# Performance work log

Hardware: AMD Instinct MI355X
Metric: run time of the kernel (lower is better)

The kernel has to match this reference:

```python
import jax, jax.numpy as jnp
import numpy as np

# Single-device reference: with head-parallel world size 1, both _SeqAllToAll
# collectives are identities, so the forward is exactly the kv-packed causal
# attention computed by loongtrain_attn_kvpacked_func (flash-attn semantics).

def setup_inputs() -> dict:
    key = jax.random.key(0)
    k1, k2 = jax.random.split(key)
    B, S, H, D = 1, 2048, 32, 128
    q = jax.random.normal(k1, (B, S, H, D), dtype=jnp.float32)
    kv = jax.random.normal(k2, (B, S, 2, H, D), dtype=jnp.float32)
    return {"q": q, "kv": kv}


def reference(q, kv) -> jnp.ndarray:
    # q: [B, S, H, D]; kv: [B, S, 2, H, D] (flash-attn kvpacked layout)
    B, S, H, D = q.shape
    k = kv[:, :, 0]  # [B, S, H, D]
    v = kv[:, :, 1]  # [B, S, H, D]
    scale = 1.0 / jnp.sqrt(jnp.asarray(D, dtype=q.dtype))
    # scores: [B, H, Sq, Sk]
    scores = jnp.einsum("bshd,bthd->bhst", q, k) * scale
    # causal mask (LoongTrain attention is causal)
    causal = jnp.tril(jnp.ones((S, S), dtype=bool))
    scores = jnp.where(causal[None, None, :, :], scores, jnp.asarray(-jnp.inf, dtype=scores.dtype))
    probs = jax.nn.softmax(scores, axis=-1)
    # context: [B, S, H, D]
    context = jnp.einsum("bhst,bthd->bshd", probs, v)
    return context
```

## Files before the change

kernel.cpp:

```cpp
#include <hip/hip_runtime.h>
#include <hip/hip_bf16.h>

typedef __bf16 bf16_t;
typedef __bf16 bf16x4 __attribute__((ext_vector_type(4)));
typedef __bf16 bf16x8 __attribute__((ext_vector_type(8)));
typedef float  f32x4  __attribute__((ext_vector_type(4)));

constexpr int S  = 2048;
constexpr int H  = 32;
constexpr int D  = 128;
constexpr int BR = 128;
constexpr int SC = 32;
constexpr int NT = S / BR;
constexpr int KSTR  = 136;
constexpr int VSTR2 = 20;

__device__ __forceinline__ bf16x8 cvt8(f32x4 lo, f32x4 hi) {
    bf16x8 r;
#pragma unroll
    for (int j = 0; j < 4; ++j) { r[j] = (bf16_t)lo[j]; r[4 + j] = (bf16_t)hi[j]; }
    return r;
}
__device__ __forceinline__ uint32_t pk2(float a, float b) {
    union { uint32_t u; bf16_t h[2]; } r;
    r.h[0] = (bf16_t)a; r.h[1] = (bf16_t)b;
    return r.u;
}

__global__ __launch_bounds__(256, 2)
void fa_fwd(const float* __restrict__ q, const float* __restrict__ kvp,
            float* __restrict__ out) {
    __shared__ __align__(16) bf16_t   Klds[2][SC * KSTR];
    __shared__ __align__(16) uint32_t Vt2[2][D * VSTR2];

    const int bx = blockIdx.x;
    const int h  = bx & 31;
    const int i  = bx >> 5;
    const int qtile = (i < 8) ? (15 - i) : (i - 8);
    const int q0    = qtile * BR;

    const int t    = threadIdx.x;
    const int w    = t >> 6;
    const int lane = t & 63;
    const int quad = lane >> 4;
    const int m    = lane & 15;

    const float sc = 0.08838834764831845f * 1.44269504088896340f;

    const int k2 = t >> 4, kc = t & 15;
    const int r0 = 2 * k2;
    const int lr0 = ((r0 >> 3) << 2) + (r0 & 3) + ((r0 & 4) ? 16 : 0);
    const size_t rowstep = (size_t)2 * H * D;
    const size_t tstep   = (size_t)SC * rowstep;
    const float* pk = kvp + (((size_t)r0 * 2 + 0) * H + h) * D + kc * 8;
    const float* pv = kvp + (((size_t)r0 * 2 + 1) * H + h) * D + kc * 8;
    const int vpos = k2 ^ ((kc & 3) << 2);

    const int qp0   = q0 + w * 32 + m;
    const int nkv   = (qtile + 1) * (BR / SC);
    const int qmaxw = q0 + w * 32 + 31;

    bf16x8 aq[2][4];
#pragma unroll
    for (int g = 0; g < 2; ++g)
#pragma unroll
        for (int c = 0; c < 4; ++c) {
            const float* p = q + ((size_t)(qp0 + g * 16) * H + h) * D + c * 32 + quad * 8;
            f32x4 lo = *(const f32x4*)p * sc;
            f32x4 hi = *(const f32x4*)(p + 4) * sc;
            aq[g][c] = cvt8(lo, hi);
        }

    f32x4 o[2][8];
#pragma unroll
    for (int g = 0; g < 2; ++g)
#pragma unroll
        for (int idx = 0; idx < 8; ++idx) o[g][idx] = (f32x4)0.f;
    float lrow[2] = {0.f, 0.f};

    f32x4 kr[2][2], vr[2][2];
    auto ldregs = [&]() {
        kr[0][0] = *(const f32x4*)pk;             kr[0][1] = *(const f32x4*)(pk + 4);
        kr[1][0] = *(const f32x4*)(pk + rowstep); kr[1][1] = *(const f32x4*)(pk + rowstep + 4);
        vr[0][0] = *(const f32x4*)pv;             vr[0][1] = *(const f32x4*)(pv + 4);
        vr[1][0] = *(const f32x4*)(pv + rowstep); vr[1][1] = *(const f32x4*)(pv + rowstep + 4);
    };
    auto stage = [&](int b) {
        *(bf16x8*)&Klds[b][lr0       * KSTR + kc * 8] = cvt8(kr[0][0], kr[0][1]);
        *(bf16x8*)&Klds[b][(lr0 + 1) * KSTR + kc * 8] = cvt8(kr[1][0], kr[1][1]);
#pragma unroll
        for (int j = 0; j < 8; ++j) {
            const int d = kc * 8 + j;
            const float a  = (j < 4) ? vr[0][0][j] : vr[0][1][j - 4];
            const float bb = (j < 4) ? vr[1][0][j] : vr[1][1][j - 4];
            Vt2[b][d * VSTR2 + vpos] = pk2(a, bb);
        }
    };

    ldregs();
    stage(0);
    if (nkv > 1) { pk += tstep; pv += tstep; ldregs(); }
    __syncthreads();

    for (int kb = 0; kb < nkv; ++kb) {
        const int kv0 = kb * SC;
        const int cur = kb & 1;
        const bool active = (kv0 <= qmaxw);

        bf16x8 bp0, bp1, av[8];
        if (active) {
            f32x4 sA[2][2];
#pragma unroll
            for (int g = 0; g < 2; ++g) { sA[g][0] = (f32x4)0.f; sA[g][1] = (f32x4)0.f; }
            __builtin_amdgcn_s_setprio(1);
#pragma unroll
            for (int c = 0; c < 4; ++c) {
                bf16x8 ak0 = *(const bf16x8*)&Klds[cur][m * KSTR + c * 32 + quad * 8];
                bf16x8 ak1 = *(const bf16x8*)&Klds[cur][(16 + m) * KSTR + c * 32 + quad * 8];
                sA[0][0] = __builtin_amdgcn_mfma_f32_16x16x32_bf16(ak0, aq[0][c], sA[0][0], 0, 0, 0);
                sA[0][1] = __builtin_amdgcn_mfma_f32_16x16x32_bf16(ak1, aq[0][c], sA[0][1], 0, 0, 0);
                sA[1][0] = __builtin_amdgcn_mfma_f32_16x16x32_bf16(ak0, aq[1][c], sA[1][0], 0, 0, 0);
                sA[1][1] = __builtin_amdgcn_mfma_f32_16x16x32_bf16(ak1, aq[1][c], sA[1][1], 0, 0, 0);
            }
            __builtin_amdgcn_s_setprio(0);

#pragma unroll
            for (int tt = 0; tt < 8; ++tt) {
                const int dd  = tt * 16 + m;
                const int grp = quad ^ ((dd >> 3) & 3);
                av[tt] = *(const bf16x8*)&Vt2[cur][dd * VSTR2 + grp * 4];
            }

#pragma unroll
            for (int g = 0; g < 2; ++g) {
                const int limb = q0 + w * 32 + g * 16 - kv0;
                float p[8], rs = 0.f;
                if (limb >= 31) {
#pragma unroll
                    for (int r = 0; r < 4; ++r) {
                        p[r]     = __builtin_amdgcn_exp2f(fminf(sA[g][0][r], 80.f));
                        p[4 + r] = __builtin_amdgcn_exp2f(fminf(sA[g][1][r], 80.f));
                        rs += p[r] + p[4 + r];
                    }
                } else {
                    const int lim = limb + m;
#pragma unroll
                    for (int r = 0; r < 4; ++r) {
                        float e0 = __builtin_amdgcn_exp2f(fminf(sA[g][0][r], 80.f));
                        float e1 = __builtin_amdgcn_exp2f(fminf(sA[g][1][r], 80.f));
                        p[r]     = (quad * 8 + r     <= lim) ? e0 : 0.f;
                        p[4 + r] = (quad * 8 + 4 + r <= lim) ? e1 : 0.f;
                        rs += p[r] + p[4 + r];
                    }
                }
                lrow[g] += rs;
                bf16x8 bv;
#pragma unroll
                for (int r = 0; r < 4; ++r) { bv[r] = (bf16_t)p[r]; bv[4 + r] = (bf16_t)p[4 + r]; }
                if (g == 0) bp0 = bv; else bp1 = bv;
            }
        }

        if (kb + 1 < nkv) {
            stage(cur ^ 1);
            if (kb + 2 < nkv) { pk += tstep; pv += tstep; ldregs(); }
        }

        if (active) {
            __builtin_amdgcn_s_setprio(1);
#pragma unroll
            for (int tt = 0; tt < 8; ++tt) {
                o[0][tt] = __builtin_amdgcn_mfma_f32_16x16x32_bf16(av[tt], bp0, o[0][tt], 0, 0, 0);
                o[1][tt] = __builtin_amdgcn_mfma_f32_16x16x32_bf16(av[tt], bp1, o[1][tt], 0, 0, 0);
            }
            __builtin_amdgcn_s_setprio(0);
        }
        __syncthreads();
    }

#pragma unroll
    for (int g = 0; g < 2; ++g) {
        lrow[g] += __shfl_xor(lrow[g], 16);
        lrow[g] += __shfl_xor(lrow[g], 32);
    }

#pragma unroll
    for (int g = 0; g < 2; ++g) {
        const float inv = 1.0f / lrow[g];
        float* op = out + ((size_t)(qp0 + g * 16) * H + h) * D;
#pragma unroll
        for (int tt = 0; tt < 8; ++tt) {
            f32x4 val = o[g][tt] * inv;
            *(f32x4*)(op + tt * 16 + quad * 4) = val;
        }
    }
}

extern "C" void kernel_launch(void* const* d_in, const int* in_sizes, int n_in,
                              void* d_out, int out_size, void* d_ws, size_t ws_size,
                              hipStream_t stream) {
    const float* q  = (const float*)d_in[0];
    const float* kv = (const float*)d_in[1];
    float* out = (float*)d_out;
    dim3 grid(NT * H);
    dim3 block(256);
    fa_fwd<<<grid, block, 0, stream>>>(q, kv, out);
}
```

Measured before the change: 176.9 us.

## Halve query tile to 64 rows, one 16-row group per wave, raise occupancy

Shrinks the query tile from 128 to 64 rows, so each wave handles a single 16-row group. This doubles the grid and allows four blocks per CU, with a new four-group interleaved tile order to balance causal work. V fragments are now loaded from LDS just before the PV MFMAs instead of being held in registers. The V transpose stores are also reordered by column half, which looks aimed at avoiding LDS bank conflicts. In exchange, each K/V chunk is reloaded and converted from fp32 by twice as many blocks, doubling global K/V traffic and staging work per unit of compute.

Measured after the change: 190.8 us. 1.08x slower.

```diff
diff --git a/kernel.cpp b/kernel.cpp
--- a/kernel.cpp
+++ b/kernel.cpp
@@ -9,7 +9,7 @@
 constexpr int S  = 2048;
 constexpr int H  = 32;
 constexpr int D  = 128;
-constexpr int BR = 128;
+constexpr int BR = 64;
 constexpr int SC = 32;
 constexpr int NT = S / BR;
 constexpr int KSTR  = 136;
@@ -27,7 +27,7 @@
     return r.u;
 }
 
-__global__ __launch_bounds__(256, 2)
+__global__ __launch_bounds__(256, 4)
 void fa_fwd(const float* __restrict__ q, const float* __restrict__ kvp,
             float* __restrict__ out) {
     __shared__ __align__(16) bf16_t   Klds[2][SC * KSTR];
@@ -36,7 +36,9 @@
     const int bx = blockIdx.x;
     const int h  = bx & 31;
     const int i  = bx >> 5;
-    const int qtile = (i < 8) ? (15 - i) : (i - 8);
+    const int jg = i & 7, gi = i >> 3;
+    const int qtile = (gi == 0) ? (31 - jg) : (gi == 1) ? jg
+                     : (gi == 2) ? (23 - jg) : (8 + jg);
     const int q0    = qtile * BR;
 
     const int t    = threadIdx.x;
@@ -55,28 +57,25 @@
     const float* pk = kvp + (((size_t)r0 * 2 + 0) * H + h) * D + kc * 8;
     const float* pv = kvp + (((size_t)r0 * 2 + 1) * H + h) * D + kc * 8;
     const int vpos = k2 ^ ((kc & 3) << 2);
+    const bool hb  = (kc & 4) != 0;
 
-    const int qp0   = q0 + w * 32 + m;
+    const int qp0   = q0 + w * 16 + m;
     const int nkv   = (qtile + 1) * (BR / SC);
-    const int qmaxw = q0 + w * 32 + 31;
+    const int qmaxw = q0 + w * 16 + 15;
 
-    bf16x8 aq[2][4];
+    bf16x8 aq[4];
 #pragma unroll
-    for (int g = 0; g < 2; ++g)
+    for (int c = 0; c < 4; ++c) {
+        const float* p = q + ((size_t)qp0 * H + h) * D + c * 32 + quad * 8;
+        f32x4 lo = *(const f32x4*)p * sc;
+        f32x4 hi = *(const f32x4*)(p + 4) * sc;
+        aq[c] = cvt8(lo, hi);
+    }
+
+    f32x4 o[8];
 #pragma unroll
-        for (int c = 0; c < 4; ++c) {
-            const float* p = q + ((size_t)(qp0 + g * 16) * H + h) * D + c * 32 + quad * 8;
-            f32x4 lo = *(const f32x4*)p * sc;
-            f32x4 hi = *(const f32x4*)(p + 4) * sc;
-            aq[g][c] = cvt8(lo, hi);
-        }
-
-    f32x4 o[2][8];
-#pragma unroll
-    for (int g = 0; g < 2; ++g)
-#pragma unroll
-        for (int idx = 0; idx < 8; ++idx) o[g][idx] = (f32x4)0.f;
-    float lrow[2] = {0.f, 0.f};
+    for (int idx = 0; idx < 8; ++idx) o[idx] = (f32x4)0.f;
+    float lrow = 0.f;
 
     f32x4 kr[2][2], vr[2][2];
     auto ldregs = [&]() {
@@ -88,12 +87,16 @@
     auto stage = [&](int b) {
         *(bf16x8*)&Klds[b][lr0       * KSTR + kc * 8] = cvt8(kr[0][0], kr[0][1]);
         *(bf16x8*)&Klds[b][(lr0 + 1) * KSTR + kc * 8] = cvt8(kr[1][0], kr[1][1]);
+        f32x4 aA = hb ? vr[0][1] : vr[0][0];
+        f32x4 bA = hb ? vr[1][1] : vr[1][0];
+        f32x4 aB = hb ? vr[0][0] : vr[0][1];
+        f32x4 bB = hb ? vr[1][0] : vr[1][1];
+        const int dA = kc * 8 + (hb ? 4 : 0);
+        const int dB = kc * 8 + (hb ? 0 : 4);
 #pragma unroll
-        for (int j = 0; j < 8; ++j) {
-            const int d = kc * 8 + j;
-            const float a  = (j < 4) ? vr[0][0][j] : vr[0][1][j - 4];
-            const float bb = (j < 4) ? vr[1][0][j] : vr[1][1][j - 4];
-            Vt2[b][d * VSTR2 + vpos] = pk2(a, bb);
+        for (int jq = 0; jq < 4; ++jq) {
+            Vt2[b][(dA + jq) * VSTR2 + vpos] = pk2(aA[jq], bA[jq]);
+            Vt2[b][(dB + jq) * VSTR2 + vpos] = pk2(aB[jq], bB[jq]);
         }
     };
 
@@ -107,58 +110,43 @@
         const int cur = kb & 1;
         const bool active = (kv0 <= qmaxw);
 
-        bf16x8 bp0, bp1, av[8];
+        bf16x8 bp;
         if (active) {
-            f32x4 sA[2][2];
-#pragma unroll
-            for (int g = 0; g < 2; ++g) { sA[g][0] = (f32x4)0.f; sA[g][1] = (f32x4)0.f; }
+            f32x4 sA[2];
+            sA[0] = (f32x4)0.f; sA[1] = (f32x4)0.f;
             __builtin_amdgcn_s_setprio(1);
 #pragma unroll
             for (int c = 0; c < 4; ++c) {
                 bf16x8 ak0 = *(const bf16x8*)&Klds[cur][m * KSTR + c * 32 + quad * 8];
                 bf16x8 ak1 = *(const bf16x8*)&Klds[cur][(16 + m) * KSTR + c * 32 + quad * 8];
-                sA[0][0] = __builtin_amdgcn_mfma_f32_16x16x32_bf16(ak0, aq[0][c], sA[0][0], 0, 0, 0);
-                sA[0][1] = __builtin_amdgcn_mfma_f32_16x16x32_bf16(ak1, aq[0][c], sA[0][1], 0, 0, 0);
-                sA[1][0] = __builtin_amdgcn_mfma_f32_16x16x32_bf16(ak0, aq[1][c], sA[1][0], 0, 0, 0);
-                sA[1][1] = __builtin_amdgcn_mfma_f32_16x16x32_bf16(ak1, aq[1][c], sA[1][1], 0, 0, 0);
+                sA[0] = __builtin_amdgcn_mfma_f32_16x16x32_bf16(ak0, aq[c], sA[0], 0, 0, 0);
+                sA[1] = __builtin_amdgcn_mfma_f32_16x16x32_bf16(ak1, aq[c], sA[1], 0, 0, 0);
             }
             __builtin_amdgcn_s_setprio(0);
 
+            const int limb = q0 + w * 16 - kv0;
+            float p[8], rs = 0.f;
+            if (limb >= 31) {
 #pragma unroll
-            for (int tt = 0; tt < 8; ++tt) {
-                const int dd  = tt * 16 + m;
-                const int grp = quad ^ ((dd >> 3) & 3);
-                av[tt] = *(const bf16x8*)&Vt2[cur][dd * VSTR2 + grp * 4];
+                for (int r = 0; r < 4; ++r) {
+                    p[r]     = __builtin_amdgcn_exp2f(fminf(sA[0][r], 80.f));
+                    p[4 + r] = __builtin_amdgcn_exp2f(fminf(sA[1][r], 80.f));
+                    rs += p[r] + p[4 + r];
+                }
+            } else {
+                const int lim = limb + m;
+#pragma unroll
+                for (int r = 0; r < 4; ++r) {
+                    float e0 = __builtin_amdgcn_exp2f(fminf(sA[0][r], 80.f));
+                    float e1 = __builtin_amdgcn_exp2f(fminf(sA[1][r], 80.f));
+                    p[r]     = (quad * 8 + r     <= lim) ? e0 : 0.f;
+                    p[4 + r] = (quad * 8 + 4 + r <= lim) ? e1 : 0.f;
+                    rs += p[r] + p[4 + r];
+                }
             }
-
+            lrow += rs;
 #pragma unroll
-            for (int g = 0; g < 2; ++g) {
-                const int limb = q0 + w * 32 + g * 16 - kv0;
-                float p[8], rs = 0.f;
-                if (limb >= 31) {
-#pragma unroll
-                    for (int r = 0; r < 4; ++r) {
-                        p[r]     = __builtin_amdgcn_exp2f(fminf(sA[g][0][r], 80.f));
-                        p[4 + r] = __builtin_amdgcn_exp2f(fminf(sA[g][1][r], 80.f));
-                        rs += p[r] + p[4 + r];
-                    }
-                } else {
-                    const int lim = limb + m;
-#pragma unroll
-                    for (int r = 0; r < 4; ++r) {
-                        float e0 = __builtin_amdgcn_exp2f(fminf(sA[g][0][r], 80.f));
-                        float e1 = __builtin_amdgcn_exp2f(fminf(sA[g][1][r], 80.f));
-                        p[r]     = (quad * 8 + r     <= lim) ? e0 : 0.f;
-                        p[4 + r] = (quad * 8 + 4 + r <= lim) ? e1 : 0.f;
-                        rs += p[r] + p[4 + r];
-                    }
-                }
-                lrow[g] += rs;
-                bf16x8 bv;
-#pragma unroll
-                for (int r = 0; r < 4; ++r) { bv[r] = (bf16_t)p[r]; bv[4 + r] = (bf16_t)p[4 + r]; }
-                if (g == 0) bp0 = bv; else bp1 = bv;
-            }
+            for (int r = 0; r < 4; ++r) { bp[r] = (bf16_t)p[r]; bp[4 + r] = (bf16_t)p[4 + r]; }
         }
 
         if (kb + 1 < nkv) {
@@ -170,27 +158,25 @@
             __builtin_amdgcn_s_setprio(1);
 #pragma unroll
             for (int tt = 0; tt < 8; ++tt) {
-                o[0][tt] = __builtin_amdgcn_mfma_f32_16x16x32_bf16(av[tt], bp0, o[0][tt], 0, 0, 0);
-                o[1][tt] = __builtin_amdgcn_mfma_f32_16x16x32_bf16(av[tt], bp1, o[1][tt], 0, 0, 0);
+                const int dd  = tt * 16 + m;
+                const int grp = quad ^ ((dd >> 3) & 3);
+                bf16x8 av = *(const bf16x8*)&Vt2[cur][dd * VSTR2 + grp * 4];
+                o[tt] = __builtin_amdgcn_mfma_f32_16x16x32_bf16(av, bp, o[tt], 0, 0, 0);
             }
             __builtin_amdgcn_s_setprio(0);
         }
         __syncthreads();
     }
 
-#pragma unroll
-    for (int g = 0; g < 2; ++g) {
-        lrow[g] += __shfl_xor(lrow[g], 16);
-        lrow[g] += __shfl_xor(lrow[g], 32);
-    }
+    lrow += __shfl_xor(lrow, 16);
+    lrow += __shfl_xor(lrow, 32);
 
-#pragma unroll
-    for (int g = 0; g < 2; ++g) {
-        const float inv = 1.0f / lrow[g];
-        float* op = out + ((size_t)(qp0 + g * 16) * H + h) * D;
+    {
+        const float inv = 1.0f / lrow;
+        float* op = out + ((size_t)qp0 * H + h) * D;
 #pragma unroll
         for (int tt = 0; tt < 8; ++tt) {
-            f32x4 val = o[g][tt] * inv;
+            f32x4 val = o[tt] * inv;
             *(f32x4*)(op + tt * 16 + quad * 4) = val;
         }
     }
```
